# Kernel tuning notes

Measured on AMD Instinct MI355X. Metric: run time of the kernel, lower is better.

## Reference

```python
import jax, jax.numpy as jnp
import numpy as np

B, S, E, D = 4, 2048, 1024, 1024
NEG_INF = float('-inf')


def setup_inputs() -> dict:
    key = jax.random.key(0)
    ks = jax.random.split(key, 10)
    query = jax.random.normal(ks[0], (B, S, E), dtype=jnp.float32)
    key_t = jax.random.normal(ks[1], (B, S, E), dtype=jnp.float32)
    value = jax.random.normal(ks[2], (B, S, E), dtype=jnp.float32)
    # Linear params (torch convention: y = x @ W.T + b)
    sc = 1.0 / np.sqrt(E)
    Wq = jax.random.uniform(ks[3], (D, E), jnp.float32, -sc, sc)
    bq = jax.random.uniform(ks[4], (D,), jnp.float32, -sc, sc)
    Wk = jax.random.uniform(ks[5], (D, E), jnp.float32, -sc, sc)
    bk = jax.random.uniform(ks[6], (D,), jnp.float32, -sc, sc)
    Wv = jax.random.uniform(ks[7], (D, E), jnp.float32, -sc, sc)
    bv = jax.random.uniform(ks[8], (D,), jnp.float32, -sc, sc)
    # padding mask: True = masked key position; ensure key 0 is never masked
    # so no row is fully -inf under the causal mask.
    lengths = jax.random.randint(ks[9], (B, 1, 1), 1, S + 1)  # valid length per batch
    pos = jnp.arange(S)[None, None, :]
    padding_mask = pos >= lengths  # [B,1,S] bool
    return {
        "query": query, "key": key_t, "value": value,
        "Wq": Wq, "bq": bq, "Wk": Wk, "bk": bk, "Wv": Wv, "bv": bv,
        "padding_mask": padding_mask, "look_ahead_mask": 1,
    }


def reference(query, key, value, Wq, bq, Wk, bk, Wv, bv, padding_mask, look_ahead_mask):
    q = query @ Wq.T + bq          # [B,S,D]
    k = key @ Wk.T + bk            # [B,S,D]
    v = value @ Wv.T + bv          # [B,S,D]
    scale = jnp.sqrt(jnp.asarray(q.shape[-1], q.dtype))
    qk = jnp.einsum('bqd,bkd->bqk', q, k) / scale  # [B,S,S]
    if padding_mask is not None:
        qk = jnp.where(padding_mask, NEG_INF, qk)
    if look_ahead_mask:
        causal = jnp.where(
            jnp.tril(jnp.ones((q.shape[1], k.shape[1]), dtype=bool)),
            jnp.asarray(0.0, qk.dtype), jnp.asarray(NEG_INF, qk.dtype))
        qk = qk + causal
    attn = jax.nn.softmax(qk, axis=-1)
    return jnp.einsum('bqk,bkd->bqd', attn, v)  # [B,S,D]
```

## Files before the change

kernel.cpp:

```cpp
#include <hip/hip_runtime.h>
#include <cstdint>
#include <cstddef>

#define B_ 4
#define S_ 2048
#define E_ 1024
#define D_ 1024
#define MFLAT (B_*S_)

typedef __attribute__((ext_vector_type(4))) float f32x4;
typedef __attribute__((ext_vector_type(8))) short short8;
typedef unsigned short u16;
typedef unsigned int   u32;

__device__ __forceinline__ u16 f2bf(float f) {
  u32 u = __float_as_uint(f);
  u = (u + 0x7fffu + ((u >> 16) & 1u)) >> 16;
  return (u16)u;
}

__device__ __forceinline__ void gll16(const void* g, void* lds) {
  __builtin_amdgcn_global_load_lds(
      (const __attribute__((address_space(1))) void*)g,
      (__attribute__((address_space(3))) void*)lds, 16, 0, 0);
}

#define BARRIER() do { asm volatile("" ::: "memory"); \
                       __builtin_amdgcn_s_barrier();  \
                       asm volatile("" ::: "memory"); } while (0)

__device__ __forceinline__ void gemm256s_core(
    const u16* __restrict__ Ag, int lda,
    const u16* __restrict__ Bg, int ldb,
    int NT, char* lds, f32x4 acc[8][4])
{
  const int tid = threadIdx.x;
  const int l = tid & 63;
  const int w = tid >> 6;
  const int wm = w >> 2, wn = w & 3;

  const int scs = (((tid & 7) ^ ((tid >> 3) & 7)) << 4);
  const char* srcA = (const char*)Ag
      + (size_t)((tid >> 8) * 128 + ((tid & 255) >> 3)) * (size_t)lda * 2 + scs;
  const char* srcB = (const char*)Bg + (size_t)(tid >> 3) * (size_t)ldb * 2 + scs;
  const size_t astep = (size_t)lda * 64;
  const size_t bstep = (size_t)ldb * 128;
  char* dA0 = lds + ((tid >> 8) << 14) + ((tid & 255) << 4);
  char* dB0 = lds + 65536 + (tid << 4);

  const int fr = l & 15, kq = l >> 4;
  const int kx = (l & 7) << 4;
  const int kc0 = (kq << 4) ^ kx;
  const int kc1 = ((kq << 4) + 64) ^ kx;
  const int aoff = (wm << 14) + fr * 128;
  const int boff = 65536 + wn * 8192 + fr * 128;

#define SG_A(q) gll16(srcA + (q)*astep + tso, dA0 + sb + (q)*4096)
#define SG_B(u) gll16(srcB + (u)*bstep + tso, dB0 + sb + (u)*8192)
#define LDA_(mf, kc) (*(const short8*)(lds + bufo + aoff + (mf)*2048 + (kc)))
#define LDB_(nf, kc) (*(const short8*)(lds + bufo + boff + (nf)*2048 + (kc)))
#define WAIT_LGKM() asm volatile("s_waitcnt lgkmcnt(0)" ::: "memory")
#define MFMA_PH(p) do {                                                          \
    __builtin_amdgcn_s_setprio(1);                                               \
    _Pragma("unroll")                                                            \
    for (int i_ = 0; i_ < 2; ++i_) {                                             \
      _Pragma("unroll")                                                          \
      for (int j_ = 0; j_ < 4; ++j_) {                                           \
        acc[2*(p)+i_][j_] = __builtin_amdgcn_mfma_f32_16x16x32_bf16(             \
            areg[i_][0], breg[j_][0], acc[2*(p)+i_][j_], 0, 0, 0);               \
        acc[2*(p)+i_][j_] = __builtin_amdgcn_mfma_f32_16x16x32_bf16(             \
            areg[i_][1], breg[j_][1], acc[2*(p)+i_][j_], 0, 0, 0);               \
      }                                                                          \
    }                                                                            \
    __builtin_amdgcn_s_setprio(0);                                               \
  } while (0)

  short8 areg[2][2], breg[4][2];

  {
    const size_t tso = 0; const int sb = 0;
    SG_B(0); SG_B(1); SG_B(2); SG_B(3);
    SG_A(0); SG_A(1); SG_A(2); SG_A(3);
  }

  for (int t = 0; t < NT; ++t) {
    const int bufo = (t & 1) << 15;
    const int sb = ((t + 1) & 1) << 15;
    const int tsi = (t + 1 == NT) ? 0 : (t + 1);
    const size_t tso = (size_t)tsi << 7;

    asm volatile("s_waitcnt vmcnt(3)" ::: "memory");
    BARRIER();
#pragma unroll
    for (int nf = 0; nf < 4; ++nf) { breg[nf][0] = LDB_(nf, kc0); breg[nf][1] = LDB_(nf, kc1); }
#pragma unroll
    for (int i = 0; i < 2; ++i) { areg[i][0] = LDA_(i, kc0); areg[i][1] = LDA_(i, kc1); }
    SG_B(0); SG_B(1);
    WAIT_LGKM();
    MFMA_PH(0);

    asm volatile("s_waitcnt vmcnt(4)" ::: "memory");
    BARRIER();
#pragma unroll
    for (int i = 0; i < 2; ++i) { areg[i][0] = LDA_(2+i, kc0); areg[i][1] = LDA_(2+i, kc1); }
    SG_B(2); SG_B(3);
    WAIT_LGKM();
    MFMA_PH(1);

    asm volatile("s_waitcnt vmcnt(5)" ::: "memory");
    BARRIER();
#pragma unroll
    for (int i = 0; i < 2; ++i) { areg[i][0] = LDA_(4+i, kc0); areg[i][1] = LDA_(4+i, kc1); }
    SG_A(0); SG_A(1);
    WAIT_LGKM();
    MFMA_PH(2);

    asm volatile("s_waitcnt vmcnt(6)" ::: "memory");
    BARRIER();
#pragma unroll
    for (int i = 0; i < 2; ++i) { areg[i][0] = LDA_(6+i, kc0); areg[i][1] = LDA_(6+i, kc1); }
    SG_A(2); SG_A(3);
    WAIT_LGKM();
    MFMA_PH(3);
  }
  asm volatile("s_waitcnt vmcnt(0)" ::: "memory");
  BARRIER();
#undef SG_A
#undef SG_B
#undef LDA_
#undef LDB_
#undef WAIT_LGKM
#undef MFMA_PH
}

__global__ __launch_bounds__(256) void cvt3_kernel(
    const float* __restrict__ s0, const float* __restrict__ s1,
    const float* __restrict__ s2, u16* __restrict__ dst, int segn4)
{
  int idx = blockIdx.x * blockDim.x + threadIdx.x;
  int stride = gridDim.x * blockDim.x;
  const int total = 3 * segn4;
  for (int i = idx; i < total; i += stride) {
    int s = i / segn4;
    int off = i - s * segn4;
    const float4* sp = (s == 0) ? (const float4*)s0 : (s == 1) ? (const float4*)s1 : (const float4*)s2;
    float4 f = sp[off];
    ushort4 o;
    o.x = f2bf(f.x); o.y = f2bf(f.y); o.z = f2bf(f.z); o.w = f2bf(f.w);
    ((ushort4*)dst)[i] = o;
  }
}

__global__ __launch_bounds__(256) void lengths_kernel(const void* __restrict__ mask,
                                                      int* __restrict__ lengths) {
  __shared__ int isbytes;
  const int t = threadIdx.x;
  if (t == 0) isbytes = 0;
  __syncthreads();
  const int* wi = (const int*)mask;
  int bad = 0;
  for (int idx = t; idx < (B_*S_)/4; idx += 256) {
    int v = wi[idx];
    if (v != 0 && v != 1) bad = 1;
  }
  if (bad) atomicOr(&isbytes, 1);
  __syncthreads();
  const int isb = isbytes;
  const int w = t >> 6, l = t & 63;
  const unsigned char* mb = (const unsigned char*)mask;
  int cnt = 0;
  for (int j = l; j < S_; j += 64) {
    int val = isb ? (int)mb[(size_t)w*S_ + j] : wi[(size_t)w*S_ + j];
    cnt += (val == 0);
  }
#pragma unroll
  for (int off = 32; off >= 1; off >>= 1) cnt += __shfl_xor(cnt, off);
  if (l == 0) lengths[w] = cnt;
}

__global__ __launch_bounds__(512, 2) void proj256_kernel(
    const u16* __restrict__ X, const u16* __restrict__ W,
    const float* __restrict__ bq, const float* __restrict__ bk, const float* __restrict__ bv,
    u16* __restrict__ q, u16* __restrict__ k, u16* __restrict__ v)
{
  extern __shared__ char lds[];
  const int bid = blockIdx.x;
  const int wg = (bid & 7) * 48 + (bid >> 3);
  const int z  = wg >> 7;
  const int rem = wg & 127;
  const int nt = rem >> 5;
  const int mt = rem & 31;

  const u16* Xz = X + (size_t)z * ((size_t)MFLAT * E_) + (size_t)(mt*256)*E_;
  const u16* Wz = W + (size_t)z * ((size_t)D_ * E_)    + (size_t)(nt*256)*E_;
  f32x4 acc[8][4];
#pragma unroll
  for (int i = 0; i < 8; ++i)
#pragma unroll
    for (int j = 0; j < 4; ++j) acc[i][j] = (f32x4){0.f,0.f,0.f,0.f};

  gemm256s_core(Xz, E_, Wz, E_, E_/64, lds, acc);

  const float* bias = (z == 0) ? bq : (z == 1) ? bk : bv;
  u16* out = (z == 0) ? q : (z == 1) ? k : v;
  const int tid = threadIdx.x, w = tid >> 6, l = tid & 63;
  const int wm = w >> 2, wn = w & 3;
  const int fr = l & 15, kq = l >> 4;
  const int orow0 = mt*256 + wm*128 + kq*4;
  const int ocol0 = nt*256 + wn*64 + fr;
#pragma unroll
  for (int nf = 0; nf < 4; ++nf) {
    const int col = ocol0 + nf*16;
    const float bcol = bias[col];
#pragma unroll
    for (int mf = 0; mf < 8; ++mf)
#pragma unroll
      for (int r = 0; r < 4; ++r)
        out[(size_t)(orow0 + mf*16 + r)*D_ + col] = f2bf(acc[mf][nf][r] + bcol);
  }
}

__global__ __launch_bounds__(256) void transpose_kernel(
    const u16* __restrict__ v, u16* __restrict__ vT)
{
  __shared__ u16 tl[64][68];
  const int xt = blockIdx.x;
  const int yt = blockIdx.y;
  const int b  = blockIdx.z;
  const int t = threadIdx.x;
  const int r0 = t >> 4;
  const int c4 = (t & 15) << 2;
  const u16* src = v + ((size_t)b*S_ + yt*64)*D_ + xt*64;
#pragma unroll
  for (int rr = r0; rr < 64; rr += 16) {
    ushort4 u = *(const ushort4*)(src + (size_t)rr*D_ + c4);
    tl[rr][c4+0] = u.x; tl[rr][c4+1] = u.y; tl[rr][c4+2] = u.z; tl[rr][c4+3] = u.w;
  }
  __syncthreads();
  u16* dst = vT + ((size_t)b*D_ + xt*64)*S_ + yt*64;
#pragma unroll
  for (int rr = r0; rr < 64; rr += 16) {
    ushort4 u;
    u.x = tl[c4+0][rr]; u.y = tl[c4+1][rr]; u.z = tl[c4+2][rr]; u.w = tl[c4+3][rr];
    *(ushort4*)(dst + (size_t)rr*S_ + c4) = u;
  }
}

__global__ __launch_bounds__(512, 2) void qk256_kernel(
    const u16* __restrict__ q, const u16* __restrict__ k,
    const int* __restrict__ lengths, float* __restrict__ scores)
{
  const int bid = blockIdx.x;
  const int wg = (bid & 7) * 18 + (bid >> 3);
  const int b = wg / 36;
  const int r = wg - b * 36;
  int ty = (int)((sqrtf(8.0f * (float)r + 1.0f) - 1.0f) * 0.5f);
  while ((ty + 1) * (ty + 2) / 2 <= r) ++ty;
  while (ty * (ty + 1) / 2 > r) --ty;
  const int tx = r - ty * (ty + 1) / 2;

  const int len = lengths[b];
  if (tx * 256 >= len) return;
  extern __shared__ char lds[];
  f32x4 acc[8][4];
#pragma unroll
  for (int i = 0; i < 8; ++i)
#pragma unroll
    for (int j = 0; j < 4; ++j) acc[i][j] = (f32x4){0.f,0.f,0.f,0.f};
  const u16* Aq = q + ((size_t)b*S_ + (size_t)ty*256) * D_;
  const u16* Bk = k + ((size_t)b*S_ + (size_t)tx*256) * D_;
  gemm256s_core(Aq, D_, Bk, D_, D_/64, lds, acc);

  const int tid = threadIdx.x, w = tid >> 6, l = tid & 63;
  const int wm = w >> 2, wn = w & 3;
  const int fr = l & 15, kq = l >> 4;
  const int orow0 = ty*256 + wm*128 + kq*4;
  const int ocol0 = tx*256 + wn*64 + fr;
  float* sb = scores + (size_t)b*S_*S_;
#pragma unroll
  for (int mf = 0; mf < 8; ++mf)
#pragma unroll
    for (int nf = 0; nf < 4; ++nf)
#pragma unroll
      for (int r2 = 0; r2 < 4; ++r2)
        sb[(size_t)(orow0 + mf*16 + r2)*S_ + (ocol0 + nf*16)] = acc[mf][nf][r2] * 0.03125f;
}

__global__ __launch_bounds__(256) void softmax_kernel(
    const float* __restrict__ scores, const int* __restrict__ lengths,
    u16* __restrict__ P)
{
  const int i = blockIdx.x, b = blockIdx.y;
  const int len = lengths[b];
  const int kmax = min(i + 1, len);
  const float* row = scores + ((size_t)b*S_ + i)*S_;
  u16* prow = P + ((size_t)b*S_ + i)*S_;
  const int t = threadIdx.x;
  const int j0 = t * 8;
  float v[8];
  {
    float4 x0 = *(const float4*)(row + j0);
    float4 x1 = *(const float4*)(row + j0 + 4);
    v[0]=x0.x; v[1]=x0.y; v[2]=x0.z; v[3]=x0.w;
    v[4]=x1.x; v[5]=x1.y; v[6]=x1.z; v[7]=x1.w;
  }
  float m = -3.4e38f;
#pragma unroll
  for (int e = 0; e < 8; ++e) if (j0 + e < kmax) m = fmaxf(m, v[e]);
#pragma unroll
  for (int off = 32; off >= 1; off >>= 1) m = fmaxf(m, __shfl_xor(m, off));
  __shared__ float redm[4], reds[4];
  if ((t & 63) == 0) redm[t >> 6] = m;
  __syncthreads();
  m = fmaxf(fmaxf(redm[0], redm[1]), fmaxf(redm[2], redm[3]));
  float s = 0.f, ex[8];
#pragma unroll
  for (int e = 0; e < 8; ++e) {
    ex[e] = (j0 + e < kmax) ? __expf(v[e] - m) : 0.f;
    s += ex[e];
  }
#pragma unroll
  for (int off = 32; off >= 1; off >>= 1) s += __shfl_xor(s, off);
  if ((t & 63) == 0) reds[t >> 6] = s;
  __syncthreads();
  s = reds[0] + reds[1] + reds[2] + reds[3];
  const float inv = 1.0f / s;
  short8 o;
#pragma unroll
  for (int e = 0; e < 8; ++e) o[e] = (short)f2bf(ex[e] * inv);
  *(short8*)(prow + j0) = o;
}

__global__ __launch_bounds__(512, 2) void pv256_kernel(
    const u16* __restrict__ P, const u16* __restrict__ vT,
    const int* __restrict__ lengths, float* __restrict__ out)
{
  extern __shared__ char lds[];
  const int bid = blockIdx.x;
  const int wg = (bid & 7) * 16 + (bid >> 3);
  const int b = wg >> 5;
  const int rem = wg & 31;
  const int ty = rem >> 2;
  const int xt = rem & 3;
  const int len = lengths[b];
  const int kend = min(ty * 256 + 256, len);
  const int NT = (kend + 63) >> 6;

  f32x4 acc[8][4];
#pragma unroll
  for (int i = 0; i < 8; ++i)
#pragma unroll
    for (int j = 0; j < 4; ++j) acc[i][j] = (f32x4){0.f,0.f,0.f,0.f};
  const u16* Ap = P  + ((size_t)b*S_ + (size_t)ty*256) * S_;
  const u16* Bv = vT + ((size_t)b*D_ + (size_t)xt*256) * S_;
  gemm256s_core(Ap, S_, Bv, S_, NT, lds, acc);

  const int tid = threadIdx.x, w = tid >> 6, l = tid & 63;
  const int wm = w >> 2, wn = w & 3;
  const int fr = l & 15, kq = l >> 4;
  const int orow0 = ty*256 + wm*128 + kq*4;
  const int ocol0 = xt*256 + wn*64 + fr;
  float* ob = out + (size_t)b*S_*D_;
#pragma unroll
  for (int mf = 0; mf < 8; ++mf)
#pragma unroll
    for (int nf = 0; nf < 4; ++nf)
#pragma unroll
      for (int r2 = 0; r2 < 4; ++r2)
        ob[(size_t)(orow0 + mf*16 + r2)*D_ + (ocol0 + nf*16)] = acc[mf][nf][r2];
}

extern "C" void kernel_launch(void* const* d_in, const int* in_sizes, int n_in,
                              void* d_out, int out_size, void* d_ws, size_t ws_size,
                              hipStream_t stream)
{
  const float* query = (const float*)d_in[0];
  const float* key_  = (const float*)d_in[1];
  const float* value = (const float*)d_in[2];
  const float* Wq = (const float*)d_in[3];
  const float* bq = (const float*)d_in[4];
  const float* Wk = (const float*)d_in[5];
  const float* bk = (const float*)d_in[6];
  const float* Wv = (const float*)d_in[7];
  const float* bv = (const float*)d_in[8];
  const void*  pmask = d_in[9];
  float* out = (float*)d_out;
  char* ws = (char*)d_ws;

  (void)hipFuncSetAttribute((const void*)proj256_kernel,
                            hipFuncAttributeMaxDynamicSharedMemorySize, 131072);
  (void)hipFuncSetAttribute((const void*)qk256_kernel,
                            hipFuncAttributeMaxDynamicSharedMemorySize, 131072);
  (void)hipFuncSetAttribute((const void*)pv256_kernel,
                            hipFuncAttributeMaxDynamicSharedMemorySize, 131072);

  int* lengths = (int*)ws;
  u16* q   = (u16*)(ws + 256);
  u16* kk  = q  + (size_t)MFLAT * D_;
  u16* vT  = kk + (size_t)MFLAT * D_;
  u16* Pbuf = (u16*)(ws + 50331904ull);
  u16* vbuf = Pbuf;
  char* scratch = ws + 83886336ull;
  u16* Xb = (u16*)scratch;
  u16* Wb = Xb + 3ull * MFLAT * E_;
  float* scores = (float*)scratch;

  cvt3_kernel<<<dim3(2048), 256, 0, stream>>>(query, key_, value, Xb, (MFLAT*E_)/4);
  cvt3_kernel<<<dim3(512),  256, 0, stream>>>(Wq, Wk, Wv, Wb, (D_*E_)/4);
  lengths_kernel<<<dim3(1), 256, 0, stream>>>(pmask, lengths);

  proj256_kernel<<<dim3(384), 512, 131072, stream>>>(Xb, Wb, bq, bk, bv, q, kk, vbuf);

  transpose_kernel<<<dim3(16, 32, 4), 256, 0, stream>>>(vbuf, vT);

  qk256_kernel<<<dim3(144), 512, 131072, stream>>>(q, kk, lengths, scores);

  softmax_kernel<<<dim3(2048, 4), 256, 0, stream>>>(scores, lengths, Pbuf);

  pv256_kernel<<<dim3(128), 512, 131072, stream>>>(Pbuf, vT, lengths, out);
}
```

Before: 345.0 us.

## Use 128x128 tiles for QK and PV GEMMs to fill more CUs

```diff
diff --git a/kernel.cpp b/kernel.cpp
--- a/kernel.cpp
+++ b/kernel.cpp
@@ -133,6 +133,81 @@
 #undef MFMA_PH
 }
 
+__device__ __forceinline__ void gemm128_core(
+    const u16* __restrict__ Ag, int lda,
+    const u16* __restrict__ Bg, int ldb,
+    int NT, char* lds, f32x4 acc[4][4])
+{
+  const int tid = threadIdx.x;
+  const int l = tid & 63;
+  const int w = tid >> 6;
+  const int wm = w >> 1, wn = w & 1;
+
+  const int scs = (((tid & 7) ^ ((tid >> 3) & 7)) << 4);
+  const char* srcA = (const char*)Ag + (size_t)(tid >> 3) * (size_t)lda * 2 + scs;
+  const char* srcB = (const char*)Bg + (size_t)(tid >> 3) * (size_t)ldb * 2 + scs;
+  const size_t asw = (size_t)lda * 64;
+  const size_t bsw = (size_t)ldb * 64;
+  char* dA0 = lds + (tid << 4);
+  char* dB0 = lds + 32768 + (tid << 4);
+
+  const int fr = l & 15, kq = l >> 4;
+  const int kx = (l & 7) << 4;
+  const int kc0 = (kq << 4) ^ kx;
+  const int kc1 = ((kq << 4) + 64) ^ kx;
+  const int aoff = wm * 8192 + fr * 128;
+  const int boff = 32768 + wn * 8192 + fr * 128;
+
+#define SG8(tk) do {                                                             \
+    const size_t ko = (size_t)(tk) << 7;                                         \
+    char* da = dA0 + sbuf; char* db = dB0 + sbuf;                                \
+    gll16(srcA + ko,           da);                                              \
+    gll16(srcA + ko +   asw,   da + 4096);                                       \
+    gll16(srcA + ko + 2*asw,   da + 8192);                                       \
+    gll16(srcA + ko + 3*asw,   da + 12288);                                      \
+    gll16(srcB + ko,           db);                                              \
+    gll16(srcB + ko +   bsw,   db + 4096);                                       \
+    gll16(srcB + ko + 2*bsw,   db + 8192);                                       \
+    gll16(srcB + ko + 3*bsw,   db + 12288);                                      \
+  } while (0)
+
+  short8 a8[4][2], b8[4][2];
+  { const int sbuf = 0; SG8(0); }
+
+  for (int t = 0; t < NT; ++t) {
+    const int bufo = (t & 1) << 14;
+    const int sbuf = ((t + 1) & 1) << 14;
+    if (t + 1 < NT) {
+      SG8(t + 1);
+      asm volatile("s_waitcnt vmcnt(8)" ::: "memory");
+    } else {
+      asm volatile("s_waitcnt vmcnt(0)" ::: "memory");
+    }
+    BARRIER();
+#pragma unroll
+    for (int mf = 0; mf < 4; ++mf) {
+      a8[mf][0] = *(const short8*)(lds + bufo + aoff + mf*2048 + kc0);
+      a8[mf][1] = *(const short8*)(lds + bufo + aoff + mf*2048 + kc1);
+    }
+#pragma unroll
+    for (int nf = 0; nf < 4; ++nf) {
+      b8[nf][0] = *(const short8*)(lds + bufo + boff + nf*2048 + kc0);
+      b8[nf][1] = *(const short8*)(lds + bufo + boff + nf*2048 + kc1);
+    }
+    __builtin_amdgcn_s_setprio(1);
+#pragma unroll
+    for (int mf = 0; mf < 4; ++mf)
+#pragma unroll
+      for (int nf = 0; nf < 4; ++nf) {
+        acc[mf][nf] = __builtin_amdgcn_mfma_f32_16x16x32_bf16(a8[mf][0], b8[nf][0], acc[mf][nf], 0, 0, 0);
+        acc[mf][nf] = __builtin_amdgcn_mfma_f32_16x16x32_bf16(a8[mf][1], b8[nf][1], acc[mf][nf], 0, 0, 0);
+      }
+    __builtin_amdgcn_s_setprio(0);
+    BARRIER();
+  }
+#undef SG8
+}
+
 __global__ __launch_bounds__(256) void cvt3_kernel(
     const float* __restrict__ s0, const float* __restrict__ s1,
     const float* __restrict__ s2, u16* __restrict__ dst, int segn4)
@@ -246,39 +321,39 @@
   }
 }
 
-__global__ __launch_bounds__(512, 2) void qk256_kernel(
+__global__ __launch_bounds__(256, 2) void qk128_kernel(
     const u16* __restrict__ q, const u16* __restrict__ k,
     const int* __restrict__ lengths, float* __restrict__ scores)
 {
   const int bid = blockIdx.x;
-  const int wg = (bid & 7) * 18 + (bid >> 3);
-  const int b = wg / 36;
-  const int r = wg - b * 36;
+  const int wg = (bid & 7) * 68 + (bid >> 3);
+  const int b = wg / 136;
+  const int r = wg - b * 136;
   int ty = (int)((sqrtf(8.0f * (float)r + 1.0f) - 1.0f) * 0.5f);
   while ((ty + 1) * (ty + 2) / 2 <= r) ++ty;
   while (ty * (ty + 1) / 2 > r) --ty;
   const int tx = r - ty * (ty + 1) / 2;
 
   const int len = lengths[b];
-  if (tx * 256 >= len) return;
+  if (tx * 128 >= len) return;
   extern __shared__ char lds[];
-  f32x4 acc[8][4];
-#pragma unroll
-  for (int i = 0; i < 8; ++i)
+  f32x4 acc[4][4];
+#pragma unroll
+  for (int i = 0; i < 4; ++i)
 #pragma unroll
     for (int j = 0; j < 4; ++j) acc[i][j] = (f32x4){0.f,0.f,0.f,0.f};
-  const u16* Aq = q + ((size_t)b*S_ + (size_t)ty*256) * D_;
-  const u16* Bk = k + ((size_t)b*S_ + (size_t)tx*256) * D_;
-  gemm256s_core(Aq, D_, Bk, D_, D_/64, lds, acc);
+  const u16* Aq = q + ((size_t)b*S_ + (size_t)ty*128) * D_;
+  const u16* Bk = k + ((size_t)b*S_ + (size_t)tx*128) * D_;
+  gemm128_core(Aq, D_, Bk, D_, D_/64, lds, acc);
 
   const int tid = threadIdx.x, w = tid >> 6, l = tid & 63;
-  const int wm = w >> 2, wn = w & 3;
+  const int wm = w >> 1, wn = w & 1;
   const int fr = l & 15, kq = l >> 4;
-  const int orow0 = ty*256 + wm*128 + kq*4;
-  const int ocol0 = tx*256 + wn*64 + fr;
+  const int orow0 = ty*128 + wm*64 + kq*4;
+  const int ocol0 = tx*128 + wn*64 + fr;
   float* sb = scores + (size_t)b*S_*S_;
 #pragma unroll
-  for (int mf = 0; mf < 8; ++mf)
+  for (int mf = 0; mf < 4; ++mf)
 #pragma unroll
     for (int nf = 0; nf < 4; ++nf)
 #pragma unroll
@@ -298,11 +373,14 @@
   const int t = threadIdx.x;
   const int j0 = t * 8;
   float v[8];
-  {
+  if (j0 < kmax) {
     float4 x0 = *(const float4*)(row + j0);
     float4 x1 = *(const float4*)(row + j0 + 4);
     v[0]=x0.x; v[1]=x0.y; v[2]=x0.z; v[3]=x0.w;
     v[4]=x1.x; v[5]=x1.y; v[6]=x1.z; v[7]=x1.w;
+  } else {
+#pragma unroll
+    for (int e = 0; e < 8; ++e) v[e] = 0.f;
   }
   float m = -3.4e38f;
 #pragma unroll
@@ -331,38 +409,38 @@
   *(short8*)(prow + j0) = o;
 }
 
-__global__ __launch_bounds__(512, 2) void pv256_kernel(
+__global__ __launch_bounds__(256, 2) void pv128_kernel(
     const u16* __restrict__ P, const u16* __restrict__ vT,
     const int* __restrict__ lengths, float* __restrict__ out)
 {
   extern __shared__ char lds[];
   const int bid = blockIdx.x;
-  const int wg = (bid & 7) * 16 + (bid >> 3);
-  const int b = wg >> 5;
-  const int rem = wg & 31;
-  const int ty = rem >> 2;
-  const int xt = rem & 3;
+  const int wg = (bid & 7) * 64 + (bid >> 3);
+  const int b = wg >> 7;
+  const int rem = wg & 127;
+  const int ty = rem >> 3;
+  const int xt = rem & 7;
   const int len = lengths[b];
-  const int kend = min(ty * 256 + 256, len);
+  const int kend = min(ty * 128 + 128, len);
   const int NT = (kend + 63) >> 6;
 
-  f32x4 acc[8][4];
-#pragma unroll
-  for (int i = 0; i < 8; ++i)
+  f32x4 acc[4][4];
+#pragma unroll
+  for (int i = 0; i < 4; ++i)
 #pragma unroll
     for (int j = 0; j < 4; ++j) acc[i][j] = (f32x4){0.f,0.f,0.f,0.f};
-  const u16* Ap = P  + ((size_t)b*S_ + (size_t)ty*256) * S_;
-  const u16* Bv = vT + ((size_t)b*D_ + (size_t)xt*256) * S_;
-  gemm256s_core(Ap, S_, Bv, S_, NT, lds, acc);
+  const u16* Ap = P  + ((size_t)b*S_ + (size_t)ty*128) * S_;
+  const u16* Bv = vT + ((size_t)b*D_ + (size_t)xt*128) * S_;
+  gemm128_core(Ap, S_, Bv, S_, NT, lds, acc);
 
   const int tid = threadIdx.x, w = tid >> 6, l = tid & 63;
-  const int wm = w >> 2, wn = w & 3;
+  const int wm = w >> 1, wn = w & 1;
   const int fr = l & 15, kq = l >> 4;
-  const int orow0 = ty*256 + wm*128 + kq*4;
-  const int ocol0 = xt*256 + wn*64 + fr;
+  const int orow0 = ty*128 + wm*64 + kq*4;
+  const int ocol0 = xt*128 + wn*64 + fr;
   float* ob = out + (size_t)b*S_*D_;
 #pragma unroll
-  for (int mf = 0; mf < 8; ++mf)
+  for (int mf = 0; mf < 4; ++mf)
 #pragma unroll
     for (int nf = 0; nf < 4; ++nf)
 #pragma unroll
@@ -389,10 +467,10 @@
 
   (void)hipFuncSetAttribute((const void*)proj256_kernel,
                             hipFuncAttributeMaxDynamicSharedMemorySize, 131072);
-  (void)hipFuncSetAttribute((const void*)qk256_kernel,
-                            hipFuncAttributeMaxDynamicSharedMemorySize, 131072);
-  (void)hipFuncSetAttribute((const void*)pv256_kernel,
-                            hipFuncAttributeMaxDynamicSharedMemorySize, 131072);
+  (void)hipFuncSetAttribute((const void*)qk128_kernel,
+                            hipFuncAttributeMaxDynamicSharedMemorySize, 65536);
+  (void)hipFuncSetAttribute((const void*)pv128_kernel,
+                            hipFuncAttributeMaxDynamicSharedMemorySize, 65536);
 
   int* lengths = (int*)ws;
   u16* q   = (u16*)(ws + 256);
@@ -413,9 +491,9 @@
 
   transpose_kernel<<<dim3(16, 32, 4), 256, 0, stream>>>(vbuf, vT);
 
-  qk256_kernel<<<dim3(144), 512, 131072, stream>>>(q, kk, lengths, scores);
+  qk128_kernel<<<dim3(544), 256, 65536, stream>>>(q, kk, lengths, scores);
 
   softmax_kernel<<<dim3(2048, 4), 256, 0, stream>>>(scores, lengths, Pbuf);
 
-  pv256_kernel<<<dim3(128), 512, 131072, stream>>>(Pbuf, vT, lengths, out);
-}
+  pv128_kernel<<<dim3(512), 256, 65536, stream>>>(Pbuf, vT, lengths, out);
+}
```

Measured after the change: 332.2 us. 1.04x faster.
